# Performance work log

Measured on AMD Instinct MI355X. Metric: run time of the kernel, lower is better.

## Reference

```python
import jax, jax.numpy as jnp
import numpy as np

N = 100000   # nodes
E = 5000000  # edges (avg degree 50)
H = 16       # hidden dim


def gcn_conv(x, edge_index, edge_weight, W, b, num_nodes):
    """PyG GCNConv with edge weights: add self-loops (weight 1), symmetric
    normalization deg^-1/2 * w * deg^-1/2, linear transform, scatter-add."""
    row, col = edge_index[0], edge_index[1]  # source j -> target i
    loop = jnp.arange(num_nodes, dtype=edge_index.dtype)
    row = jnp.concatenate([row, loop])
    col = jnp.concatenate([col, loop])
    w = jnp.concatenate([edge_weight, jnp.ones((num_nodes,), edge_weight.dtype)])
    deg = jax.ops.segment_sum(w, col, num_segments=num_nodes)
    dinv = jnp.where(deg > 0, jax.lax.rsqrt(jnp.where(deg > 0, deg, 1.0)), 0.0)
    norm = dinv[row] * w * dinv[col]               # [E+N]
    h = x @ W                                      # [N, out]
    msg = norm[:, None] * h[row]                   # gather + scale
    out = jax.ops.segment_sum(msg, col, num_segments=num_nodes)  # scatter-add
    return out + b


def setup_inputs() -> dict:
    key = jax.random.key(0)
    k = jax.random.split(key, 7)
    x = jax.random.normal(k[0], (N, 1), dtype=jnp.float32)
    edge_index = jax.random.randint(k[1], (2, E), 0, N, dtype=jnp.int32)
    edge_attr = jax.random.uniform(k[2], (E,), dtype=jnp.float32)
    W1 = jax.random.normal(k[3], (1, H), dtype=jnp.float32) * (1.0 / np.sqrt(1.0))
    b1 = jnp.zeros((H,), dtype=jnp.float32)
    W2 = jax.random.normal(k[4], (H, 1), dtype=jnp.float32) * (1.0 / np.sqrt(H))
    b2 = jnp.zeros((1,), dtype=jnp.float32)
    return {"x": x, "edge_index": edge_index, "edge_attr": edge_attr,
            "W1": W1, "b1": b1, "W2": W2, "b2": b2}


def reference(x, edge_index, edge_attr, W1, b1, W2, b2):
    h = gcn_conv(x, edge_index, edge_attr, W1, b1, N)
    h = jax.nn.relu(h)
    out = gcn_conv(h, edge_index, edge_attr, W2, b2, N)
    return out
```

## Files before the change

### kernel.cpp

```cpp
#include <hip/hip_runtime.h>

#define T       256
#define BSHIFT  12
#define BSIZE   4096
#define MAXNB   32
#define M       32
#define EPB     4096
#define EPT     (EPB / T)

__global__ void k_count(const int* __restrict__ col, int* __restrict__ cntT,
                        int E, int nb, int ebp) {
    __shared__ int hist[MAXNB];
    int t = threadIdx.x, g = blockIdx.x;
    if (t < MAXNB) hist[t] = 0;
    __syncthreads();
    int base = g * EPB;
    bool full = (base + EPB <= E);
    if (full) {
#pragma unroll
        for (int k = 0; k < EPT / 4; ++k) {
            int4 c = *(const int4*)(col + base + (t + k * T) * 4);
            atomicAdd(&hist[c.x >> BSHIFT], 1);
            atomicAdd(&hist[c.y >> BSHIFT], 1);
            atomicAdd(&hist[c.z >> BSHIFT], 1);
            atomicAdd(&hist[c.w >> BSHIFT], 1);
        }
    } else {
        for (int k = 0; k < EPT; ++k) {
            int e = base + t + k * T;
            if (e < E) atomicAdd(&hist[col[e] >> BSHIFT], 1);
        }
    }
    __syncthreads();
    if (t < nb) cntT[t * ebp + g] = hist[t];
}

__global__ void k_scan(const int* __restrict__ cntT, int* __restrict__ ofsT,
                       int* __restrict__ tot, int eb, int ebp) {
    __shared__ int tsum[T];
    __shared__ int carry;
    int b = blockIdx.x, t = threadIdx.x;
    if (t == 0) carry = 0;
    __syncthreads();
    int rounds = (eb + T - 1) / T;
    for (int jr = 0; jr < rounds; ++jr) {
        int idx = jr * T + t;
        int v = (idx < eb) ? cntT[b * ebp + idx] : 0;
        tsum[t] = v;
        __syncthreads();
        for (int d = 1; d < T; d <<= 1) {
            int o = (t >= d) ? tsum[t - d] : 0;
            __syncthreads();
            tsum[t] += o;
            __syncthreads();
        }
        int excl = tsum[t] - v + carry;
        if (idx < eb) ofsT[b * ebp + idx] = excl;
        __syncthreads();
        if (t == 0) carry += tsum[T - 1];
        __syncthreads();
    }
    if (t == 0) tot[b] = carry;
}

__global__ void k_scatter(const int* __restrict__ row, const int* __restrict__ col,
                          const float* __restrict__ w,
                          const int* __restrict__ cntT, const int* __restrict__ ofsT,
                          const int* __restrict__ tot,
                          int2* __restrict__ rec, int E, int nb, int ebp) {
    __shared__ int  lofs[MAXNB + 1];
    __shared__ int  rnk[MAXNB];
    __shared__ int  rbase[MAXNB];
    __shared__ int2 buf[EPB];
    __shared__ unsigned char bkt[EPB];
    int t = threadIdx.x, g = blockIdx.x;
    if (t < MAXNB) rnk[t] = 0;
    if (t < 64) {
        int tv = (t < nb) ? ((tot[t] + 3) & ~3) : 0;
        int incA = tv;
#pragma unroll
        for (int d = 1; d < 32; d <<= 1) {
            int o = __shfl_up(incA, d, 64);
            if (t >= d) incA += o;
        }
        int h = (t < nb) ? cntT[t * ebp + g] : 0;
        int incB = h;
#pragma unroll
        for (int d = 1; d < 32; d <<= 1) {
            int o = __shfl_up(incB, d, 64);
            if (t >= d) incB += o;
        }
        if (t == 0) lofs[0] = 0;
        if (t < nb) {
            lofs[t + 1] = incB;
            rbase[t] = (incA - tv) + ofsT[t * ebp + g];
        }
    }
    __syncthreads();

    int base = g * EPB;
    bool full = (base + EPB <= E);
    if (full) {
#pragma unroll
        for (int k = 0; k < EPT / 4; ++k) {
            int idx = base + (t + k * T) * 4;
            int4   c  = *(const int4*)(col + idx);
            int4   r  = *(const int4*)(row + idx);
            float4 wv = *(const float4*)(w + idx);
            int b, rk, pos;
            b = c.x >> BSHIFT; rk = atomicAdd(&rnk[b], 1); pos = lofs[b] + rk;
            buf[pos] = make_int2(((c.x & (BSIZE-1)) << 17) | r.x, __float_as_int(wv.x));
            bkt[pos] = (unsigned char)b;
            b = c.y >> BSHIFT; rk = atomicAdd(&rnk[b], 1); pos = lofs[b] + rk;
            buf[pos] = make_int2(((c.y & (BSIZE-1)) << 17) | r.y, __float_as_int(wv.y));
            bkt[pos] = (unsigned char)b;
            b = c.z >> BSHIFT; rk = atomicAdd(&rnk[b], 1); pos = lofs[b] + rk;
            buf[pos] = make_int2(((c.z & (BSIZE-1)) << 17) | r.z, __float_as_int(wv.z));
            bkt[pos] = (unsigned char)b;
            b = c.w >> BSHIFT; rk = atomicAdd(&rnk[b], 1); pos = lofs[b] + rk;
            buf[pos] = make_int2(((c.w & (BSIZE-1)) << 17) | r.w, __float_as_int(wv.w));
            bkt[pos] = (unsigned char)b;
        }
    } else {
        for (int k = 0; k < EPT; ++k) {
            int e = base + t + k * T;
            if (e < E) {
                int c = col[e];
                int b = c >> BSHIFT;
                int rk = atomicAdd(&rnk[b], 1);
                int pos = lofs[b] + rk;
                buf[pos] = make_int2(((c & (BSIZE-1)) << 17) | row[e], __float_as_int(w[e]));
                bkt[pos] = (unsigned char)b;
            }
        }
    }
    __syncthreads();
    int total = lofs[nb];
    for (int j = t; j < total; j += T) {
        int b = bkt[j];
        rec[rbase[b] + (j - lofs[b])] = buf[j];
    }
}

template <bool HAS_SRC>
__global__ void k_acc(const int2* __restrict__ rec, const int* __restrict__ tot,
                      const float* __restrict__ src, float* __restrict__ part, int nb) {
    __shared__ float acc[BSIZE];
    __shared__ int   bst[MAXNB];
    int t = threadIdx.x, g = blockIdx.x;
    int b = g / M, m = g % M;
    if (t < 64) {
        int tv = (t < nb) ? ((tot[t] + 3) & ~3) : 0;
        int inc = tv;
#pragma unroll
        for (int d = 1; d < 32; d <<= 1) {
            int o = __shfl_up(inc, d, 64);
            if (t >= d) inc += o;
        }
        if (t < nb) bst[t] = inc - tv;
    }
    for (int j = t; j < BSIZE; j += T) acc[j] = 0.0f;
    __syncthreads();
    int s  = bst[b];
    int tb = tot[b];
    int chunk = ((tb + M - 1) / M + 7) & ~7;
    int lo = s + m * chunk;
    int hi = min(s + tb, lo + chunk);
    const int4* rec4 = (const int4*)rec;
    int i = lo + t * 8;
    for (; i + 7 < hi; i += T * 8) {
        int4 q0 = rec4[(i >> 1) + 0];
        int4 q1 = rec4[(i >> 1) + 1];
        int4 q2 = rec4[(i >> 1) + 2];
        int4 q3 = rec4[(i >> 1) + 3];
        float v0 = __int_as_float(q0.y), v1 = __int_as_float(q0.w);
        float v2 = __int_as_float(q1.y), v3 = __int_as_float(q1.w);
        float v4 = __int_as_float(q2.y), v5 = __int_as_float(q2.w);
        float v6 = __int_as_float(q3.y), v7 = __int_as_float(q3.w);
        if (HAS_SRC) {
            v0 *= src[q0.x & 0x1FFFF]; v1 *= src[q0.z & 0x1FFFF];
            v2 *= src[q1.x & 0x1FFFF]; v3 *= src[q1.z & 0x1FFFF];
            v4 *= src[q2.x & 0x1FFFF]; v5 *= src[q2.z & 0x1FFFF];
            v6 *= src[q3.x & 0x1FFFF]; v7 *= src[q3.z & 0x1FFFF];
        }
        atomicAdd(&acc[((unsigned)q0.x) >> 17], v0);
        atomicAdd(&acc[((unsigned)q0.z) >> 17], v1);
        atomicAdd(&acc[((unsigned)q1.x) >> 17], v2);
        atomicAdd(&acc[((unsigned)q1.z) >> 17], v3);
        atomicAdd(&acc[((unsigned)q2.x) >> 17], v4);
        atomicAdd(&acc[((unsigned)q2.z) >> 17], v5);
        atomicAdd(&acc[((unsigned)q3.x) >> 17], v6);
        atomicAdd(&acc[((unsigned)q3.z) >> 17], v7);
    }
    for (; i < hi; ++i) {
        int2 r = rec[i];
        float v = __int_as_float(r.y);
        if (HAS_SRC) v *= src[r.x & 0x1FFFF];
        atomicAdd(&acc[((unsigned)r.x) >> 17], v);
    }
    __syncthreads();
    float* dst = part + (size_t)g * BSIZE;
    for (int j = t; j < BSIZE; j += T) dst[j] = acc[j];
}

__device__ __forceinline__ float reduceM(const float* __restrict__ part, int n) {
    int b = n >> BSHIFT, o = n & (BSIZE - 1);
    const float* pp = part + (size_t)b * M * BSIZE + o;
    float s = 0.0f;
#pragma unroll
    for (int m = 0; m < M; ++m) s += pp[(size_t)m * BSIZE];
    return s;
}

__global__ void k_red_dinv(const float* __restrict__ part, const float* __restrict__ x,
                           float* __restrict__ dinv, float* __restrict__ p, int N) {
    int i = blockIdx.x * blockDim.x + threadIdx.x;
    if (i < N) {
        float d  = reduceM(part, i) + 1.0f;
        float di = rsqrtf(d);
        dinv[i] = di;
        p[i] = di * x[i];
    }
}

__global__ void k_red_mlp(const float* __restrict__ part, const float* __restrict__ dinv,
                          const float* __restrict__ p,
                          const float* __restrict__ W1, const float* __restrict__ b1,
                          const float* __restrict__ W2,
                          float* __restrict__ q, int N) {
    int i = blockIdx.x * blockDim.x + threadIdx.x;
    if (i < N) {
        float di = dinv[i];
        float s  = di * reduceM(part, i) + di * p[i];
        float acc = 0.0f;
#pragma unroll
        for (int k = 0; k < 16; ++k) {
            float h = fmaxf(s * W1[k] + b1[k], 0.0f);
            acc += h * W2[k];
        }
        q[i] = di * acc;
    }
}

__global__ void k_red_out(const float* __restrict__ part, const float* __restrict__ dinv,
                          const float* __restrict__ q, const float* __restrict__ b2,
                          float* __restrict__ out, int N) {
    int i = blockIdx.x * blockDim.x + threadIdx.x;
    if (i < N) {
        float di = dinv[i];
        out[i] = di * reduceM(part, i) + di * q[i] + b2[0];
    }
}

extern "C" void kernel_launch(void* const* d_in, const int* in_sizes, int n_in,
                              void* d_out, int out_size, void* d_ws, size_t ws_size,
                              hipStream_t stream) {
    const float* x  = (const float*)d_in[0];
    const int*   ei = (const int*)  d_in[1];
    const float* ew = (const float*)d_in[2];
    const float* W1 = (const float*)d_in[3];
    const float* b1 = (const float*)d_in[4];
    const float* W2 = (const float*)d_in[5];
    const float* b2 = (const float*)d_in[6];

    const int N = in_sizes[0];
    const int E = in_sizes[2];
    const int* row = ei;
    const int* col = ei + E;
    const int nb  = (N + BSIZE - 1) >> BSHIFT;
    const int eb  = (E + EPB - 1) / EPB;
    const int ebp = (eb + 63) & ~63;

    char* wsp = (char*)d_ws;
    auto take = [&](size_t bytes) {
        char* r = wsp; wsp += (bytes + 255) & ~(size_t)255; return (void*)r;
    };
    int2*  rec  = (int2*) take((size_t)(E + 4 * MAXNB) * 8);
    float* part = (float*)take((size_t)nb * M * BSIZE * 4);
    float* dinv = (float*)take((size_t)N * 4);
    float* p    = (float*)take((size_t)N * 4);
    float* q    = (float*)take((size_t)N * 4);
    int*   cntT = (int*)  take((size_t)MAXNB * ebp * 4);
    int*   ofsT = (int*)  take((size_t)MAXNB * ebp * 4);
    int*   tot  = (int*)  take(MAXNB * 4);

    float* out = (float*)d_out;

    const int nbk = (N + T - 1) / T;
    const int ab  = nb * M;

    k_count  <<<eb, T, 0, stream>>>(col, cntT, E, nb, ebp);
    k_scan   <<<nb, T, 0, stream>>>(cntT, ofsT, tot, eb, ebp);
    k_scatter<<<eb, T, 0, stream>>>(row, col, ew, cntT, ofsT, tot, rec, E, nb, ebp);

    k_acc<false><<<ab, T, 0, stream>>>(rec, tot, nullptr, part, nb);
    k_red_dinv  <<<nbk, T, 0, stream>>>(part, x, dinv, p, N);

    k_acc<true><<<ab, T, 0, stream>>>(rec, tot, p, part, nb);
    k_red_mlp  <<<nbk, T, 0, stream>>>(part, dinv, p, W1, b1, W2, q, N);

    k_acc<true><<<ab, T, 0, stream>>>(rec, tot, q, part, nb);
    k_red_out  <<<nbk, T, 0, stream>>>(part, dinv, q, b2, out, N);
}
```

Baseline: 238.9 us.

## Fuse per-bucket reductions into accumulation kernels via last-block-done counters

Drops the three separate reduction kernels. Each accumulation block now bumps a per-bucket atomic counter once its partial is written, and the last block to finish for that bucket sums the M partials and applies the stage epilogue (dinv, MLP, or output). The counters are zeroed inside k_count. This removes three kernel launches and lets the reductions overlap with other buckets' accumulation, but the final reduction for each bucket runs in a single block and needs threadfences.

```diff
diff --git a/kernel.cpp b/kernel.cpp
--- a/kernel.cpp
+++ b/kernel.cpp
@@ -9,9 +9,10 @@
 #define EPT     (EPB / T)
 
 __global__ void k_count(const int* __restrict__ col, int* __restrict__ cntT,
-                        int E, int nb, int ebp) {
+                        int* __restrict__ doneAll, int E, int nb, int ebp) {
     __shared__ int hist[MAXNB];
     int t = threadIdx.x, g = blockIdx.x;
+    if (g == 0 && t < 3 * MAXNB) doneAll[t] = 0;
     if (t < MAXNB) hist[t] = 0;
     __syncthreads();
     int base = g * EPB;
@@ -142,11 +143,19 @@
     }
 }
 
-template <bool HAS_SRC>
+template <int STAGE>
 __global__ void k_acc(const int2* __restrict__ rec, const int* __restrict__ tot,
-                      const float* __restrict__ src, float* __restrict__ part, int nb) {
+                      float* __restrict__ part, int* __restrict__ done,
+                      const float* __restrict__ x,
+                      float* __restrict__ dinv, float* __restrict__ p,
+                      float* __restrict__ q,
+                      const float* __restrict__ W1, const float* __restrict__ b1,
+                      const float* __restrict__ W2, const float* __restrict__ b2,
+                      float* __restrict__ out, int N, int nb) {
     __shared__ float acc[BSIZE];
     __shared__ int   bst[MAXNB];
+    __shared__ int   tick;
+    const float* src = (STAGE == 1) ? p : ((STAGE == 2) ? q : nullptr);
     int t = threadIdx.x, g = blockIdx.x;
     int b = g / M, m = g % M;
     if (t < 64) {
@@ -177,7 +186,7 @@
         float v2 = __int_as_float(q1.y), v3 = __int_as_float(q1.w);
         float v4 = __int_as_float(q2.y), v5 = __int_as_float(q2.w);
         float v6 = __int_as_float(q3.y), v7 = __int_as_float(q3.w);
-        if (HAS_SRC) {
+        if (STAGE != 0) {
             v0 *= src[q0.x & 0x1FFFF]; v1 *= src[q0.z & 0x1FFFF];
             v2 *= src[q1.x & 0x1FFFF]; v3 *= src[q1.z & 0x1FFFF];
             v4 *= src[q2.x & 0x1FFFF]; v5 *= src[q2.z & 0x1FFFF];
@@ -195,60 +204,45 @@
     for (; i < hi; ++i) {
         int2 r = rec[i];
         float v = __int_as_float(r.y);
-        if (HAS_SRC) v *= src[r.x & 0x1FFFF];
+        if (STAGE != 0) v *= src[r.x & 0x1FFFF];
         atomicAdd(&acc[((unsigned)r.x) >> 17], v);
     }
     __syncthreads();
     float* dst = part + (size_t)g * BSIZE;
     for (int j = t; j < BSIZE; j += T) dst[j] = acc[j];
-}
-
-__device__ __forceinline__ float reduceM(const float* __restrict__ part, int n) {
-    int b = n >> BSHIFT, o = n & (BSIZE - 1);
-    const float* pp = part + (size_t)b * M * BSIZE + o;
-    float s = 0.0f;
-#pragma unroll
-    for (int m = 0; m < M; ++m) s += pp[(size_t)m * BSIZE];
-    return s;
-}
-
-__global__ void k_red_dinv(const float* __restrict__ part, const float* __restrict__ x,
-                           float* __restrict__ dinv, float* __restrict__ p, int N) {
-    int i = blockIdx.x * blockDim.x + threadIdx.x;
-    if (i < N) {
-        float d  = reduceM(part, i) + 1.0f;
-        float di = rsqrtf(d);
-        dinv[i] = di;
-        p[i] = di * x[i];
-    }
-}
-
-__global__ void k_red_mlp(const float* __restrict__ part, const float* __restrict__ dinv,
-                          const float* __restrict__ p,
-                          const float* __restrict__ W1, const float* __restrict__ b1,
-                          const float* __restrict__ W2,
-                          float* __restrict__ q, int N) {
-    int i = blockIdx.x * blockDim.x + threadIdx.x;
-    if (i < N) {
-        float di = dinv[i];
-        float s  = di * reduceM(part, i) + di * p[i];
-        float acc = 0.0f;
-#pragma unroll
-        for (int k = 0; k < 16; ++k) {
-            float h = fmaxf(s * W1[k] + b1[k], 0.0f);
-            acc += h * W2[k];
-        }
-        q[i] = di * acc;
-    }
-}
-
-__global__ void k_red_out(const float* __restrict__ part, const float* __restrict__ dinv,
-                          const float* __restrict__ q, const float* __restrict__ b2,
-                          float* __restrict__ out, int N) {
-    int i = blockIdx.x * blockDim.x + threadIdx.x;
-    if (i < N) {
-        float di = dinv[i];
-        out[i] = di * reduceM(part, i) + di * q[i] + b2[0];
+
+    __threadfence();
+    if (t == 0) tick = atomicAdd(&done[b], 1);
+    __syncthreads();
+    if (tick != M - 1) return;
+    __threadfence();
+    int nodebase = b << BSHIFT;
+    for (int j = t; j < BSIZE; j += T) {
+        int n = nodebase + j;
+        if (n >= N) break;
+        const float* pp = part + (size_t)b * M * BSIZE + j;
+        float ssum = 0.0f;
+#pragma unroll
+        for (int mm = 0; mm < M; ++mm) ssum += pp[(size_t)mm * BSIZE];
+        if (STAGE == 0) {
+            float d  = ssum + 1.0f;
+            float di = rsqrtf(d);
+            dinv[n] = di;
+            p[n] = di * x[n];
+        } else if (STAGE == 1) {
+            float di = dinv[n];
+            float sv = di * ssum + di * p[n];
+            float a = 0.0f;
+#pragma unroll
+            for (int k = 0; k < 16; ++k) {
+                float h = fmaxf(sv * W1[k] + b1[k], 0.0f);
+                a += h * W2[k];
+            }
+            q[n] = di * a;
+        } else {
+            float di = dinv[n];
+            out[n] = di * ssum + di * q[n] + b2[0];
+        }
     }
 }
 
@@ -283,22 +277,19 @@
     int*   cntT = (int*)  take((size_t)MAXNB * ebp * 4);
     int*   ofsT = (int*)  take((size_t)MAXNB * ebp * 4);
     int*   tot  = (int*)  take(MAXNB * 4);
+    int*   done = (int*)  take(3 * MAXNB * 4);
 
     float* out = (float*)d_out;
-
-    const int nbk = (N + T - 1) / T;
-    const int ab  = nb * M;
-
-    k_count  <<<eb, T, 0, stream>>>(col, cntT, E, nb, ebp);
+    const int ab = nb * M;
+
+    k_count  <<<eb, T, 0, stream>>>(col, cntT, done, E, nb, ebp);
     k_scan   <<<nb, T, 0, stream>>>(cntT, ofsT, tot, eb, ebp);
     k_scatter<<<eb, T, 0, stream>>>(row, col, ew, cntT, ofsT, tot, rec, E, nb, ebp);
 
-    k_acc<false><<<ab, T, 0, stream>>>(rec, tot, nullptr, part, nb);
-    k_red_dinv  <<<nbk, T, 0, stream>>>(part, x, dinv, p, N);
-
-    k_acc<true><<<ab, T, 0, stream>>>(rec, tot, p, part, nb);
-    k_red_mlp  <<<nbk, T, 0, stream>>>(part, dinv, p, W1, b1, W2, q, N);
-
-    k_acc<true><<<ab, T, 0, stream>>>(rec, tot, q, part, nb);
-    k_red_out  <<<nbk, T, 0, stream>>>(part, dinv, q, b2, out, N);
-}
+    k_acc<0><<<ab, T, 0, stream>>>(rec, tot, part, done + 0 * MAXNB,
+                                   x, dinv, p, q, W1, b1, W2, b2, out, N, nb);
+    k_acc<1><<<ab, T, 0, stream>>>(rec, tot, part, done + 1 * MAXNB,
+                                   x, dinv, p, q, W1, b1, W2, b2, out, N, nb);
+    k_acc<2><<<ab, T, 0, stream>>>(rec, tot, part, done + 2 * MAXNB,
+                                   x, dinv, p, q, W1, b1, W2, b2, out, N, nb);
+}
```

New measurement: 540.0 us. +126.0%, slower.
